# Kernel optimization log

Hardware: AMD Instinct MI355X
Metric: run time of the kernel (lower is better)

The kernel has to match this reference:

```python
import jax, jax.numpy as jnp
import numpy as np

EPS = 1e-5
B, S, D, H, DK, F, L, K = 2, 256, 1024, 8, 128, 4096, 8, 37


def ln(x, g, b):
    m = x.mean(-1, keepdims=True)
    v = jnp.var(x, axis=-1, keepdims=True)
    return (x - m) / jnp.sqrt(v + EPS) * g + b


def setup_inputs() -> dict:
    key = jax.random.key(0)
    ks = jax.random.split(key, 16)

    def w(k, shape):
        return jax.random.normal(k, shape, jnp.float32) * 0.02

    return {
        "x": jax.random.normal(ks[0], (B, S, D), jnp.float32),
        "relation": jax.random.randint(ks[1], (B, S, S), 0, K),
        "mask": jnp.ones((B, 1, S), jnp.bool_),
        "Wq": w(ks[2], (L, D, D)), "bq": jnp.zeros((L, D), jnp.float32),
        "Wk": w(ks[3], (L, D, D)), "bk": jnp.zeros((L, D), jnp.float32),
        "Wv": w(ks[4], (L, D, D)), "bv": jnp.zeros((L, D), jnp.float32),
        "Wo": w(ks[5], (L, D, D)), "bo": jnp.zeros((L, D), jnp.float32),
        "ln1_g": jnp.ones((L, D), jnp.float32), "ln1_b": jnp.zeros((L, D), jnp.float32),
        "W1": w(ks[6], (L, D, F)), "b1": jnp.zeros((L, F), jnp.float32),
        "W2": w(ks[7], (L, F, D)), "b2": jnp.zeros((L, D), jnp.float32),
        "ln2_g": jnp.ones((L, D), jnp.float32), "ln2_b": jnp.zeros((L, D), jnp.float32),
        "rel_k": w(ks[8], (L, K, DK)),
        "rel_v": w(ks[9], (L, K, DK)),
        "lnf_g": jnp.ones((D,), jnp.float32), "lnf_b": jnp.zeros((D,), jnp.float32),
    }


def reference(x, relation, mask, Wq, bq, Wk, bk, Wv, bv, Wo, bo, ln1_g, ln1_b,
              W1, b1, W2, b2, ln2_g, ln2_b, rel_k, rel_v, lnf_g, lnf_b):
    scale = 1.0 / np.sqrt(DK).astype(np.float32)
    maskb = mask[:, None]  # [B,1,1,S] broadcast over heads/query

    def layer(h_in, p):
        (wq, bq_, wk, bk_, wv, bv_, wo, bo_, g1, be1, w1, bf1, w2, bf2,
         g2, be2, rke, rve) = p
        h = ln(h_in, g1, be1)
        rk = rke[relation]  # [B,S,S,DK]
        rv = rve[relation]  # [B,S,S,DK]
        q = (h @ wq + bq_).reshape(B, S, H, DK).transpose(0, 2, 1, 3)
        k = (h @ wk + bk_).reshape(B, S, H, DK).transpose(0, 2, 1, 3)
        v = (h @ wv + bv_).reshape(B, S, H, DK).transpose(0, 2, 1, 3)
        scores = (jnp.einsum('bhqd,bhkd->bhqk', q, k)
                  + jnp.einsum('bhqd,bqkd->bhqk', q, rk)) * scale
        scores = jnp.where(maskb, scores, jnp.float32(-1e9))
        p_attn = jax.nn.softmax(scores, axis=-1)
        o = (jnp.einsum('bhqk,bhkd->bhqd', p_attn, v)
             + jnp.einsum('bhqk,bqkd->bhqd', p_attn, rv))
        o = o.transpose(0, 2, 1, 3).reshape(B, S, D)
        h_in = h_in + o @ wo + bo_
        h2 = ln(h_in, g2, be2)
        h_in = h_in + jax.nn.relu(h2 @ w1 + bf1) @ w2 + bf2
        return h_in, None

    xs = (Wq, bq, Wk, bk, Wv, bv, Wo, bo, ln1_g, ln1_b, W1, b1, W2, b2,
          ln2_g, ln2_b, rel_k, rel_v)
    out, _ = jax.lax.scan(layer, x, xs)
    return ln(out, lnf_g, lnf_b)
```

## Files before the change

kernel.cpp:

```cpp
#include <hip/hip_runtime.h>
#include <hip/hip_bf16.h>

typedef __hip_bfloat16 bf16;
typedef __attribute__((ext_vector_type(8))) short short8;
typedef __attribute__((ext_vector_type(4))) float f32x4;
typedef __attribute__((ext_vector_type(4))) int  int4v;

constexpr int Bc = 2, Sc = 256, Dc = 1024, Hc = 8, DKc = 128, Fc = 4096, Lc = 8, Kc = 37;
constexpr float SCALE = 0.08838834764831845f;

#define WAITV4 asm volatile("s_waitcnt vmcnt(4)" ::: "memory")
#define WAITV0 asm volatile("s_waitcnt vmcnt(0)" ::: "memory")
#define SBAR() do { __builtin_amdgcn_sched_barrier(0); __builtin_amdgcn_s_barrier(); } while (0)

__global__ __launch_bounds__(256) void detect_k(const unsigned short* __restrict__ w,
                                                int* __restrict__ flag) {
    __shared__ int cnt;
    if (threadIdx.x == 0) cnt = 0;
    __syncthreads();
    int ok = 0;
    #pragma unroll
    for (int j = 0; j < 16; j++) {
        unsigned short u = w[threadIdx.x * 16 + j];
        int e = (u >> 7) & 0xFF;
        ok += (e >= 100 && e <= 131) ? 1 : 0;
    }
    atomicAdd(&cnt, ok);
    __syncthreads();
    if (threadIdx.x == 0) *flag = (cnt < 3500) ? 1 : 0;
}

__device__ __forceinline__ float ldf(const void* p, size_t i, bool f32) {
    return f32 ? ((const float*)p)[i] : __bfloat162float(((const bf16*)p)[i]);
}

__device__ __forceinline__ void gld16(const bf16* g, bf16* l) {
    __builtin_amdgcn_global_load_lds((const __attribute__((address_space(1))) void*)g,
                                     (__attribute__((address_space(3))) void*)l, 16, 0, 0);
}

__global__ __launch_bounds__(256) void cast_k(const void* __restrict__ x, float* __restrict__ h,
                                              const int* __restrict__ flagp) {
    bool f32 = (*flagp != 0);
    size_t i = (size_t)blockIdx.x * 256 + threadIdx.x;
    h[i] = ldf(x, i, f32);
}

__global__ __launch_bounds__(256) void ln_k(const float* __restrict__ in,
                                            const void* __restrict__ g, size_t goff,
                                            const void* __restrict__ be, size_t boff,
                                            void* __restrict__ out, int outExt,
                                            const int* __restrict__ flagp) {
    bool f32 = (*flagp != 0);
    int row = blockIdx.x, tid = threadIdx.x;
    const float* rp = in + (size_t)row * Dc;
    float4 v = *(const float4*)(rp + tid * 4);
    float s  = v.x + v.y + v.z + v.w;
    float sq = v.x * v.x + v.y * v.y + v.z * v.z + v.w * v.w;
    int w = tid >> 6, lane = tid & 63;
    #pragma unroll
    for (int off = 32; off >= 1; off >>= 1) {
        s  += __shfl_down(s, off);
        sq += __shfl_down(sq, off);
    }
    __shared__ float rs[4], rq[4];
    if (lane == 0) { rs[w] = s; rq[w] = sq; }
    __syncthreads();
    float S4 = rs[0] + rs[1] + rs[2] + rs[3];
    float Q4 = rq[0] + rq[1] + rq[2] + rq[3];
    float mean = S4 * (1.f / Dc);
    float var  = Q4 * (1.f / Dc) - mean * mean;
    float rstd = rsqrtf(var + 1e-5f);
    #pragma unroll
    for (int j = 0; j < 4; j++) {
        int c = tid * 4 + j;
        float xv = (&v.x)[j];
        float val = (xv - mean) * rstd * ldf(g, goff + c, f32) + ldf(be, boff + c, f32);
        size_t idx = (size_t)row * Dc + c;
        if (outExt && f32) ((float*)out)[idx] = val;
        else               ((bf16*)out)[idx] = __float2bfloat16(val);
    }
}

__global__ __launch_bounds__(256) void conv_k(const void* __restrict__ Wq, const void* __restrict__ Wk,
                                              const void* __restrict__ Wv, const void* __restrict__ Wo,
                                              const void* __restrict__ W1, const void* __restrict__ W2,
                                              const void* __restrict__ rk, const void* __restrict__ rv,
                                              char* __restrict__ slotBase, size_t slotStride,
                                              int layer0, int slotMul,
                                              const int* __restrict__ flagp) {
    bool f32 = (*flagp != 0);
    int l = layer0 + blockIdx.y;
    char* sp = slotBase + (size_t)(slotMul ? l : 0) * slotStride;
    bf16* Wqkv_t = (bf16*)sp;
    bf16* Wo_t   = (bf16*)(sp + (6ll << 20));
    bf16* W1_t   = (bf16*)(sp + (8ll << 20));
    bf16* W2_t   = (bf16*)(sp + (16ll << 20));
    bf16* rkb    = (bf16*)(sp + (24ll << 20));
    bf16* rvt    = (bf16*)(sp + (24ll << 20) + 16384);
    size_t wOff = (size_t)l * Dc * Dc, w1Off = (size_t)l * Dc * Fc, rOff = (size_t)l * Kc * DKc;

    int bid = blockIdx.x, tid = threadIdx.x;
    if (bid == 768) {
        for (int idx = tid; idx < 64 * DKc; idx += 256) {
            int rr = idx >> 7, d = idx & 127;
            rkb[idx] = (rr < Kc) ? __float2bfloat16(ldf(rk, rOff + (size_t)rr * DKc + d, f32))
                                 : __float2bfloat16(0.f);
        }
        for (int idx = tid; idx < DKc * 64; idx += 256) {
            int d = idx >> 6, rr = idx & 63;
            rvt[idx] = (rr < Kc) ? __float2bfloat16(ldf(rv, rOff + (size_t)rr * DKc + d, f32))
                                 : __float2bfloat16(0.f);
        }
        return;
    }
    const void* src; bf16* dst; int ldn, ldk, k0, n0;
    if (bid < 256) {
        int m = bid >> 6, t = bid & 63;
        k0 = (t >> 2) * 64; n0 = (t & 3) * 256;
        src = (m == 0) ? Wq : (m == 1) ? Wk : (m == 2) ? Wv : Wo;
        src = (const void*)((const char*)src + wOff * (f32 ? 4 : 2));
        dst = (m < 3) ? (Wqkv_t + (size_t)m * Dc * Dc) : Wo_t;
        ldn = Dc; ldk = Dc;
    } else if (bid < 512) {
        int t = bid - 256;
        k0 = (t >> 4) * 64; n0 = (t & 15) * 256;
        src = (const void*)((const char*)W1 + w1Off * (f32 ? 4 : 2));
        dst = W1_t; ldn = Fc; ldk = Dc;
    } else {
        int t = bid - 512;
        k0 = (t >> 2) * 64; n0 = (t & 3) * 256;
        src = (const void*)((const char*)W2 + w1Off * (f32 ? 4 : 2));
        dst = W2_t; ldn = Dc; ldk = Fc;
    }
    __shared__ bf16 sT[64][264];
    int r = tid >> 2, seg = tid & 3;
    if (f32) {
        const float* sp2 = (const float*)src + (size_t)(k0 + r) * ldn + n0 + seg * 64;
        #pragma unroll
        for (int c4 = 0; c4 < 4; c4++) {
            alignas(16) bf16 tmp[16];
            #pragma unroll
            for (int q = 0; q < 4; q++) {
                float4 fv = *(const float4*)(sp2 + c4 * 16 + q * 4);
                tmp[q * 4 + 0] = __float2bfloat16(fv.x);
                tmp[q * 4 + 1] = __float2bfloat16(fv.y);
                tmp[q * 4 + 2] = __float2bfloat16(fv.z);
                tmp[q * 4 + 3] = __float2bfloat16(fv.w);
            }
            *(int4v*)&sT[r][seg * 64 + c4 * 16]     = *(int4v*)tmp;
            *(int4v*)&sT[r][seg * 64 + c4 * 16 + 8] = *(int4v*)(tmp + 8);
        }
    } else {
        const bf16* sp2 = (const bf16*)src + (size_t)(k0 + r) * ldn + n0 + seg * 64;
        #pragma unroll
        for (int c4 = 0; c4 < 4; c4++) {
            *(int4v*)&sT[r][seg * 64 + c4 * 16]     = *(const int4v*)(sp2 + c4 * 16);
            *(int4v*)&sT[r][seg * 64 + c4 * 16 + 8] = *(const int4v*)(sp2 + c4 * 16 + 8);
        }
    }
    __syncthreads();
    alignas(16) bf16 outv[64];
    #pragma unroll
    for (int k = 0; k < 64; k++) outv[k] = sT[k][tid];
    bf16* dp = dst + (size_t)(n0 + tid) * ldk + k0;
    #pragma unroll
    for (int q = 0; q < 8; q++) *(int4v*)(dp + q * 8) = *(int4v*)(outv + q * 8);
}

__device__ __forceinline__ short8 frd(const bf16* s, int row, int g) {
    return *(const short8*)(s + (size_t)row * 64 + ((g ^ (row & 7)) << 3));
}

template <int MODE>
__global__ __launch_bounds__(256) void gemm2_k(const bf16* __restrict__ Ag, int lda,
                                               const bf16* __restrict__ Bt, int ldb,
                                               const void* __restrict__ bA, const void* __restrict__ bB,
                                               const void* __restrict__ bC, size_t boff,
                                               float* __restrict__ outf,
                                               bf16* __restrict__ outb, bf16* __restrict__ vtp,
                                               int N, int Kd, int nx, int znum,
                                               const int* __restrict__ flagp) {
    bool f32e = (*flagp != 0);
    __shared__ bf16 sA[3][64][64];
    __shared__ bf16 sB[3][64][64];
    int tid = threadIdx.x, wv = tid >> 6, lane = tid & 63;

    int bid = blockIdx.x;
    int c = bid & 7, j = bid >> 3;
    int npc = nx >> 3;
    int mz = 8 * znum;
    int nl = j / mz; int rem = j - nl * mz;
    int mtile = rem / znum; int kslice = rem - mtile * znum;
    int ntile = c * npc + nl;

    int row0 = mtile * 64, col0 = ntile * 64;
    const bf16* Ab = Ag + (size_t)kslice * Kd;
    const bf16* Bb = Bt + (size_t)kslice * Kd;
    int wm = (wv >> 1) * 32, wn = (wv & 1) * 32;
    int lr = lane >> 3;
    int gsw = ((lane & 7) ^ lr) * 8;
    f32x4 acc[2][2] = {};
    int nt = Kd / 64;

    auto stage = [&](int buf, int t) {
        #pragma unroll
        for (int cc = 0; cc < 2; ++cc) {
            int rr = 16 * wv + 8 * cc;
            gld16(Ab + (size_t)(row0 + rr + lr) * lda + t * 64 + gsw, &sA[buf][rr][0]);
            gld16(Bb + (size_t)(col0 + rr + lr) * ldb + t * 64 + gsw, &sB[buf][rr][0]);
        }
    };
    stage(0, 0);
    if (nt > 1) { stage(1, 1); WAITV4; } else { WAITV0; }
    SBAR();

    int r16 = lane & 15, kq = lane >> 4;
    for (int t = 0; t < nt; ++t) {
        if (t + 2 < nt) stage((t + 2) % 3, t + 2);
        int cb = t % 3;
        const bf16* pa = &sA[cb][0][0];
        const bf16* pb = &sB[cb][0][0];
        #pragma unroll
        for (int ks = 0; ks < 2; ks++) {
            int g = ks * 4 + kq;
            short8 a0 = frd(pa, wm + r16, g);
            short8 a1 = frd(pa, wm + 16 + r16, g);
            short8 b0 = frd(pb, wn + r16, g);
            short8 b1 = frd(pb, wn + 16 + r16, g);
            acc[0][0] = __builtin_amdgcn_mfma_f32_16x16x32_bf16(a0, b0, acc[0][0], 0, 0, 0);
            acc[0][1] = __builtin_amdgcn_mfma_f32_16x16x32_bf16(a0, b1, acc[0][1], 0, 0, 0);
            acc[1][0] = __builtin_amdgcn_mfma_f32_16x16x32_bf16(a1, b0, acc[1][0], 0, 0, 0);
            acc[1][1] = __builtin_amdgcn_mfma_f32_16x16x32_bf16(a1, b1, acc[1][1], 0, 0, 0);
        }
        if (t + 2 < nt) { WAITV4; } else if (t + 1 < nt) { WAITV0; }
        SBAR();
    }

    #pragma unroll
    for (int mi = 0; mi < 2; mi++) {
        #pragma unroll
        for (int ni = 0; ni < 2; ni++) {
            int col = col0 + wn + ni * 16 + r16;
            if (MODE == 0) {
                int sel = col >> 10;
                const void* bp = (sel == 0) ? bA : (sel == 1) ? bB : bC;
                float bias = ldf(bp, boff + (col & 1023), f32e);
                if (sel < 2) {
                    #pragma unroll
                    for (int r = 0; r < 4; r++) {
                        int row = row0 + wm + mi * 16 + kq * 4 + r;
                        outb[(size_t)row * 3072 + col] = __float2bfloat16(acc[mi][ni][r] + bias);
                    }
                } else {
                    int hh = (col - 2048) >> 7, d = (col - 2048) & 127;
                    int b = row0 >> 8;
                    int s0 = (row0 & 255) + wm + mi * 16 + kq * 4;
                    alignas(8) bf16 pk[4];
                    #pragma unroll
                    for (int r = 0; r < 4; r++) pk[r] = __float2bfloat16(acc[mi][ni][r] + bias);
                    *(short4*)(vtp + (((size_t)(b * 8 + hh)) * 128 + d) * 256 + s0) = *(short4*)pk;
                }
            } else if (MODE == 1) {
                float bias = ldf(bA, boff + col, f32e);
                #pragma unroll
                for (int r = 0; r < 4; r++) {
                    int row = row0 + wm + mi * 16 + kq * 4 + r;
                    float tv = acc[mi][ni][r] + bias;
                    outb[(size_t)row * N + col] = __float2bfloat16(tv > 0.f ? tv : 0.f);
                }
            } else {
                float add = (kslice == 0) ? ldf(bA, boff + col, f32e) : 0.f;
                #pragma unroll
                for (int r = 0; r < 4; r++) {
                    int row = row0 + wm + mi * 16 + kq * 4 + r;
                    atomicAdd(&outf[(size_t)row * N + col], acc[mi][ni][r] + add);
                }
            }
        }
    }
}

__global__ __launch_bounds__(64) void attn_k(const bf16* __restrict__ qkv,
                                             const bf16* __restrict__ vt,
                                             const bf16* __restrict__ rkb,
                                             const bf16* __restrict__ rvt,
                                             const int* __restrict__ relation,
                                             bf16* __restrict__ ob) {
    int z = blockIdx.y, b = z >> 3, h = z & 7;
    int q0 = blockIdx.x * 16;
    int lane = threadIdx.x;
    int l15 = lane & 15, l4 = lane >> 4;

    __shared__ float qr_s[16][48];
    __shared__ float bins_s[16][40];
    __shared__ bf16  Pl[16][264];
    __shared__ bf16  binb[16][64];

    for (int c = lane; c < 16 * 40; c += 64) bins_s[c / 40][c % 40] = 0.f;

    short8 qf[4];
    const bf16* qp = qkv + (size_t)(b * Sc + q0 + l15) * 3072 + h * DKc + l4 * 8;
    #pragma unroll
    for (int ks = 0; ks < 4; ks++) qf[ks] = *(const short8*)(qp + ks * 32);

    f32x4 sc[19];
    #pragma unroll
    for (int f = 0; f < 19; f++) sc[f] = f32x4{0.f, 0.f, 0.f, 0.f};
    const bf16* kbase = qkv + (size_t)(b * Sc) * 3072 + Dc + h * DKc;
    #pragma unroll
    for (int f = 0; f < 16; f++) {
        #pragma unroll
        for (int ks = 0; ks < 4; ks++) {
            short8 kv = *(const short8*)(kbase + (size_t)(f * 16 + l15) * 3072 + ks * 32 + l4 * 8);
            sc[f] = __builtin_amdgcn_mfma_f32_16x16x32_bf16(qf[ks], kv, sc[f], 0, 0, 0);
        }
    }
    #pragma unroll
    for (int f = 0; f < 3; f++) {
        #pragma unroll
        for (int ks = 0; ks < 4; ks++) {
            short8 rv_ = *(const short8*)(rkb + (size_t)(f * 16 + l15) * DKc + ks * 32 + l4 * 8);
            sc[16 + f] = __builtin_amdgcn_mfma_f32_16x16x32_bf16(qf[ks], rv_, sc[16 + f], 0, 0, 0);
        }
    }
    #pragma unroll
    for (int f = 0; f < 3; f++)
        #pragma unroll
        for (int r = 0; r < 4; r++)
            qr_s[l4 * 4 + r][f * 16 + l15] = sc[16 + f][r];
    __syncthreads();

    unsigned relpk[16];
    #pragma unroll
    for (int f = 0; f < 16; f++) {
        unsigned pk = 0;
        #pragma unroll
        for (int r = 0; r < 4; r++) {
            int rowl = l4 * 4 + r;
            int col = f * 16 + l15;
            int rel = relation[((size_t)b * Sc + q0 + rowl) * Sc + col];
            pk |= (unsigned)rel << (8 * r);
            sc[f][r] = (sc[f][r] + qr_s[rowl][rel]) * SCALE;
        }
        relpk[f] = pk;
    }
    float inv[4];
    #pragma unroll
    for (int r = 0; r < 4; r++) {
        float m = -3.0e38f;
        #pragma unroll
        for (int f = 0; f < 16; f++) m = fmaxf(m, sc[f][r]);
        m = fmaxf(m, __shfl_xor(m, 1)); m = fmaxf(m, __shfl_xor(m, 2));
        m = fmaxf(m, __shfl_xor(m, 4)); m = fmaxf(m, __shfl_xor(m, 8));
        float s = 0.f;
        #pragma unroll
        for (int f = 0; f < 16; f++) { float e = __expf(sc[f][r] - m); sc[f][r] = e; s += e; }
        s += __shfl_xor(s, 1); s += __shfl_xor(s, 2); s += __shfl_xor(s, 4); s += __shfl_xor(s, 8);
        inv[r] = 1.f / s;
    }
    #pragma unroll
    for (int f = 0; f < 16; f++) {
        #pragma unroll
        for (int r = 0; r < 4; r++) {
            int rowl = l4 * 4 + r;
            int col = f * 16 + l15;
            float p = sc[f][r] * inv[r];
            Pl[rowl][col] = __float2bfloat16(p);
            int rel = (relpk[f] >> (8 * r)) & 0xFF;
            atomicAdd(&bins_s[rowl][rel], p);
        }
    }
    __syncthreads();
    for (int c = lane; c < 16 * 64; c += 64) {
        int row = c >> 6, k = c & 63;
        binb[row][k] = __float2bfloat16((k < Kc) ? bins_s[row][k] : 0.f);
    }
    __syncthreads();

    f32x4 acc_o[8];
    #pragma unroll
    for (int df = 0; df < 8; df++) acc_o[df] = f32x4{0.f, 0.f, 0.f, 0.f};
    const bf16* vbase = vt + (size_t)z * DKc * Sc;
    #pragma unroll
    for (int ks = 0; ks < 8; ks++) {
        short8 af = *(const short8*)&Pl[l15][ks * 32 + l4 * 8];
        #pragma unroll
        for (int df = 0; df < 8; df++) {
            short8 bv = *(const short8*)(vbase + (size_t)(df * 16 + l15) * Sc + ks * 32 + l4 * 8);
            acc_o[df] = __builtin_amdgcn_mfma_f32_16x16x32_bf16(af, bv, acc_o[df], 0, 0, 0);
        }
    }
    #pragma unroll
    for (int ks = 0; ks < 2; ks++) {
        short8 af = *(const short8*)&binb[l15][ks * 32 + l4 * 8];
        #pragma unroll
        for (int df = 0; df < 8; df++) {
            short8 bv = *(const short8*)(rvt + (size_t)(df * 16 + l15) * 64 + ks * 32 + l4 * 8);
            acc_o[df] = __builtin_amdgcn_mfma_f32_16x16x32_bf16(af, bv, acc_o[df], 0, 0, 0);
        }
    }
    #pragma unroll
    for (int df = 0; df < 8; df++) {
        int col = df * 16 + l15;
        #pragma unroll
        for (int r = 0; r < 4; r++) {
            int rowl = l4 * 4 + r;
            ob[((size_t)(b * Sc + q0 + rowl) * Hc + h) * DKc + col] = __float2bfloat16(acc_o[df][r]);
        }
    }
}

extern "C" void kernel_launch(void* const* d_in, const int* in_sizes, int n_in,
                              void* d_out, int out_size, void* d_ws, size_t ws_size,
                              hipStream_t stream) {
    const void* x        = d_in[0];
    const int*  relation = (const int*)d_in[1];
    const void* Wq = d_in[3];  const void* bq = d_in[4];
    const void* Wk = d_in[5];  const void* bk = d_in[6];
    const void* Wv = d_in[7];  const void* bv = d_in[8];
    const void* Wo = d_in[9];  const void* bo = d_in[10];
    const void* g1 = d_in[11]; const void* be1 = d_in[12];
    const void* W1 = d_in[13]; const void* b1 = d_in[14];
    const void* W2 = d_in[15]; const void* b2 = d_in[16];
    const void* g2 = d_in[17]; const void* be2 = d_in[18];
    const void* relk = d_in[19]; const void* relv = d_in[20];
    const void* lnfg = d_in[21]; const void* lnfb = d_in[22];

    char* ws = (char*)d_ws;
    float* h    = (float*)(ws);
    bf16*  hn   = (bf16*)(ws + (2ll  << 20));
    bf16*  qkv  = (bf16*)(ws + (3ll  << 20));
    bf16*  vt   = (bf16*)(ws + (6ll  << 20));
    bf16*  ob   = (bf16*)(ws + (7ll  << 20));
    bf16*  f1   = (bf16*)(ws + (8ll  << 20));
    int*   flag = (int*)(ws + (12ll << 20));
    const size_t WBASE = 13ll << 20;
    const size_t WSTRIDE = 25ll << 20;
    int nslot = (ws_size >= WBASE + 8 * WSTRIDE) ? 8 : 1;
    char* slotBase = ws + WBASE;

    const int M = Bc * Sc;

    detect_k<<<1, 256, 0, stream>>>((const unsigned short*)Wq, flag);
    cast_k<<<(Bc * Sc * Dc) / 256, 256, 0, stream>>>(x, h, flag);

    if (nslot == 8)
        conv_k<<<dim3(769, 8), 256, 0, stream>>>(Wq, Wk, Wv, Wo, W1, W2, relk, relv,
                                                 slotBase, WSTRIDE, 0, 1, flag);

    for (int l = 0; l < Lc; l++) {
        if (nslot == 1)
            conv_k<<<dim3(769, 1), 256, 0, stream>>>(Wq, Wk, Wv, Wo, W1, W2, relk, relv,
                                                     slotBase, WSTRIDE, l, 0, flag);
        char* sp = slotBase + (size_t)((nslot == 8) ? l : 0) * WSTRIDE;
        bf16* Wqkv_t = (bf16*)sp;
        bf16* Wo_t   = (bf16*)(sp + (6ll << 20));
        bf16* W1_t   = (bf16*)(sp + (8ll << 20));
        bf16* W2_t   = (bf16*)(sp + (16ll << 20));
        bf16* rkb    = (bf16*)(sp + (24ll << 20));
        bf16* rvt    = (bf16*)(sp + (24ll << 20) + 16384);
        size_t dOff = (size_t)l * Dc, fOff = (size_t)l * Fc;

        ln_k<<<M, 256, 0, stream>>>(h, g1, dOff, be1, dOff, hn, 0, flag);

        gemm2_k<0><<<384, 256, 0, stream>>>(hn, Dc, Wqkv_t, Dc, bq, bk, bv, dOff,
                                            nullptr, qkv, vt, 3072, Dc, 48, 1, flag);

        attn_k<<<dim3(16, 16), 64, 0, stream>>>(qkv, vt, rkb, rvt, relation, ob);

        gemm2_k<2><<<512, 256, 0, stream>>>(ob, Dc, Wo_t, Dc, bo, nullptr, nullptr, dOff,
                                            h, nullptr, nullptr, Dc, 256, 16, 4, flag);

        ln_k<<<M, 256, 0, stream>>>(h, g2, dOff, be2, dOff, hn, 0, flag);

        gemm2_k<1><<<512, 256, 0, stream>>>(hn, Dc, W1_t, Dc, b1, nullptr, nullptr, fOff,
                                            nullptr, f1, nullptr, Fc, Dc, 64, 1, flag);

        gemm2_k<2><<<512, 256, 0, stream>>>(f1, Fc, W2_t, Fc, b2, nullptr, nullptr, dOff,
                                            h, nullptr, nullptr, Dc, 1024, 16, 4, flag);
    }

    ln_k<<<M, 256, 0, stream>>>(h, lnfg, 0, lnfb, 0, d_out, 1, flag);
}
```

Measured before the change: 883.2 us.

## Store converted weights in pre-swizzled contiguous 64x64 tiles for GEMM B loads

The weight conversion kernel now writes the transposed bf16 weights as contiguous 64x64 tiles (8KB each), already XOR-swizzled to match the shared-memory layout. The GEMM B-operand loads then read each tile as one contiguous block instead of 64 strided rows. This is meant to improve DRAM/L2 locality and coalescing of the weight stream, which dominates these small-M GEMMs. It changes the layout contract between the conversion and GEMM kernels, so every consumer of those buffers must use the new tile indexing.

```diff
diff --git a/kernel.cpp b/kernel.cpp
--- a/kernel.cpp
+++ b/kernel.cpp
@@ -114,24 +114,24 @@
         }
         return;
     }
-    const void* src; bf16* dst; int ldn, ldk, k0, n0;
+    const void* src; bf16* dst; int ldn, k0, n0, KT;
     if (bid < 256) {
         int m = bid >> 6, t = bid & 63;
         k0 = (t >> 2) * 64; n0 = (t & 3) * 256;
         src = (m == 0) ? Wq : (m == 1) ? Wk : (m == 2) ? Wv : Wo;
         src = (const void*)((const char*)src + wOff * (f32 ? 4 : 2));
         dst = (m < 3) ? (Wqkv_t + (size_t)m * Dc * Dc) : Wo_t;
-        ldn = Dc; ldk = Dc;
+        ldn = Dc; KT = 16;
     } else if (bid < 512) {
         int t = bid - 256;
         k0 = (t >> 4) * 64; n0 = (t & 15) * 256;
         src = (const void*)((const char*)W1 + w1Off * (f32 ? 4 : 2));
-        dst = W1_t; ldn = Fc; ldk = Dc;
+        dst = W1_t; ldn = Fc; KT = 16;
     } else {
         int t = bid - 512;
         k0 = (t >> 2) * 64; n0 = (t & 3) * 256;
         src = (const void*)((const char*)W2 + w1Off * (f32 ? 4 : 2));
-        dst = W2_t; ldn = Dc; ldk = Fc;
+        dst = W2_t; ldn = Dc; KT = 64;
     }
     __shared__ bf16 sT[64][264];
     int r = tid >> 2, seg = tid & 3;
@@ -160,12 +160,15 @@
         }
     }
     __syncthreads();
+    int nt_i = tid >> 6, n = tid & 63;
+    bf16* tileB = dst + ((((size_t)(n0 >> 6) + nt_i) * KT + (k0 >> 6)) << 12);
     alignas(16) bf16 outv[64];
     #pragma unroll
     for (int k = 0; k < 64; k++) outv[k] = sT[k][tid];
-    bf16* dp = dst + (size_t)(n0 + tid) * ldk + k0;
-    #pragma unroll
-    for (int q = 0; q < 8; q++) *(int4v*)(dp + q * 8) = *(int4v*)(outv + q * 8);
+    bf16* dp = tileB + n * 64;
+    #pragma unroll
+    for (int g = 0; g < 8; g++)
+        *(int4v*)(dp + ((g ^ (n & 7)) << 3)) = *(int4v*)(outv + g * 8);
 }
 
 __device__ __forceinline__ short8 frd(const bf16* s, int row, int g) {
@@ -174,7 +177,7 @@
 
 template <int MODE>
 __global__ __launch_bounds__(256) void gemm2_k(const bf16* __restrict__ Ag, int lda,
-                                               const bf16* __restrict__ Bt, int ldb,
+                                               const bf16* __restrict__ Bt, int KT,
                                                const void* __restrict__ bA, const void* __restrict__ bB,
                                                const void* __restrict__ bC, size_t boff,
                                                float* __restrict__ outf,
@@ -194,21 +197,23 @@
     int mtile = rem / znum; int kslice = rem - mtile * znum;
     int ntile = c * npc + nl;
 
-    int row0 = mtile * 64, col0 = ntile * 64;
+    int row0 = mtile * 64;
+    int nt = Kd / 64;
     const bf16* Ab = Ag + (size_t)kslice * Kd;
-    const bf16* Bb = Bt + (size_t)kslice * Kd;
+    const bf16* Bbase = Bt + (((size_t)ntile * KT + (size_t)kslice * nt) << 12);
     int wm = (wv >> 1) * 32, wn = (wv & 1) * 32;
     int lr = lane >> 3;
     int gsw = ((lane & 7) ^ lr) * 8;
+    int lc8 = (lane & 7) * 8;
     f32x4 acc[2][2] = {};
-    int nt = Kd / 64;
 
     auto stage = [&](int buf, int t) {
+        const bf16* bt = Bbase + ((size_t)t << 12);
         #pragma unroll
         for (int cc = 0; cc < 2; ++cc) {
             int rr = 16 * wv + 8 * cc;
             gld16(Ab + (size_t)(row0 + rr + lr) * lda + t * 64 + gsw, &sA[buf][rr][0]);
-            gld16(Bb + (size_t)(col0 + rr + lr) * ldb + t * 64 + gsw, &sB[buf][rr][0]);
+            gld16(bt + (size_t)(rr + lr) * 64 + lc8, &sB[buf][rr][0]);
         }
     };
     stage(0, 0);
@@ -237,6 +242,7 @@
         SBAR();
     }
 
+    int col0 = ntile * 64;
     #pragma unroll
     for (int mi = 0; mi < 2; mi++) {
         #pragma unroll
@@ -464,20 +470,20 @@
 
         ln_k<<<M, 256, 0, stream>>>(h, g1, dOff, be1, dOff, hn, 0, flag);
 
-        gemm2_k<0><<<384, 256, 0, stream>>>(hn, Dc, Wqkv_t, Dc, bq, bk, bv, dOff,
+        gemm2_k<0><<<384, 256, 0, stream>>>(hn, Dc, Wqkv_t, 16, bq, bk, bv, dOff,
                                             nullptr, qkv, vt, 3072, Dc, 48, 1, flag);
 
         attn_k<<<dim3(16, 16), 64, 0, stream>>>(qkv, vt, rkb, rvt, relation, ob);
 
-        gemm2_k<2><<<512, 256, 0, stream>>>(ob, Dc, Wo_t, Dc, bo, nullptr, nullptr, dOff,
+        gemm2_k<2><<<512, 256, 0, stream>>>(ob, Dc, Wo_t, 16, bo, nullptr, nullptr, dOff,
                                             h, nullptr, nullptr, Dc, 256, 16, 4, flag);
 
         ln_k<<<M, 256, 0, stream>>>(h, g2, dOff, be2, dOff, hn, 0, flag);
 
-        gemm2_k<1><<<512, 256, 0, stream>>>(hn, Dc, W1_t, Dc, b1, nullptr, nullptr, fOff,
+        gemm2_k<1><<<512, 256, 0, stream>>>(hn, Dc, W1_t, 16, b1, nullptr, nullptr, fOff,
                                             nullptr, f1, nullptr, Fc, Dc, 64, 1, flag);
 
-        gemm2_k<2><<<512, 256, 0, stream>>>(f1, Fc, W2_t, Fc, b2, nullptr, nullptr, dOff,
+        gemm2_k<2><<<512, 256, 0, stream>>>(f1, Fc, W2_t, 64, b2, nullptr, nullptr, dOff,
                                             h, nullptr, nullptr, Dc, 1024, 16, 4, flag);
     }
 
```

Measured after the change: 862.7 us, median of 2. 2.3% less time.
